# Optimization experiments

Hardware: AMD Instinct MI355X
Metric: run time of the kernel (lower is better)

The kernel has to match this reference:

```python
import jax, jax.numpy as jnp
import numpy as np

ITEM_NUM = 100000
EMBED = 128
HIDDEN = 256
BETA = 0.5
B = 4096
H = 200

def setup_inputs() -> dict:
    key = jax.random.key(0)
    ks = jax.random.split(key, 7)
    history = jax.random.randint(ks[0], (B, H), 0, ITEM_NUM)
    target = jax.random.randint(ks[1], (B,), 0, ITEM_NUM)
    embed_history = jax.random.normal(ks[2], (ITEM_NUM, EMBED), dtype=jnp.float32) * 0.01
    embed_target = jax.random.normal(ks[3], (ITEM_NUM, EMBED), dtype=jnp.float32) * 0.01
    # nn.Linear default init: U(-1/sqrt(fan_in), 1/sqrt(fan_in)); biases zeroed by _init_weight_
    lim1 = 1.0 / np.sqrt(EMBED)
    W1 = jax.random.uniform(ks[4], (EMBED, HIDDEN), dtype=jnp.float32, minval=-lim1, maxval=lim1)
    b1 = jnp.zeros((HIDDEN,), dtype=jnp.float32)
    lim2 = 1.0 / np.sqrt(HIDDEN)
    w2 = jax.random.uniform(ks[5], (HIDDEN,), dtype=jnp.float32, minval=-lim2, maxval=lim2)
    return {"history": history, "target": target, "embed_history": embed_history,
            "embed_target": embed_target, "W1": W1, "b1": b1, "w2": w2}

def reference(history, target, embed_history, embed_target, W1, b1, w2):
    hist_e = embed_history[history]            # [B, H, d]
    tgt_e = embed_target[target][:, None, :]   # [B, 1, d]
    x = hist_e * tgt_e                          # [B, H, d]
    a = jnp.einsum('bhk,k->bh', jax.nn.relu(jnp.einsum('bhd,dk->bhk', x, W1) + b1), w2)  # [B, H]
    mask = (history != target[:, None]).astype(a.dtype)  # [B, H]
    exp_A = jnp.exp(a) * mask                  # [B, H]
    denom = jnp.sum(exp_A, axis=-1) ** BETA    # [B], beta-power normalization (not softmax)
    attn = exp_A / denom[:, None]              # [B, H]
    pred = jnp.einsum('bh,bhd,bd->b', attn, hist_e, tgt_e[:, 0, :])  # [B]
    return jax.nn.sigmoid(pred)
```

## Files before the change

### kernel.cpp

```cpp
#include <hip/hip_runtime.h>

#define B_SZ   4096
#define H_SZ   200
#define D_SZ   128
#define N_SZ   256
#define ROWS   (B_SZ * H_SZ)
#define BM     64
#define TPB    8
#define RPB    (BM * TPB)
#define NBLK   (ROWS / RPB)

typedef _Float16 f16;
typedef __attribute__((ext_vector_type(2))) _Float16 f16x2;
typedef __attribute__((ext_vector_type(8))) _Float16 f16x8;
typedef __attribute__((ext_vector_type(4))) float f32x4;

union H8 { f16x8 v; f16x2 p[4]; uint4 u; };

__device__ __forceinline__ f16x2 pkrtz(float a, float b) {
    return __builtin_bit_cast(f16x2, __builtin_amdgcn_cvt_pkrtz(a, b));
}

__global__ __launch_bounds__(256) void cvt_eh(const float* __restrict__ src,
                                              uint4* __restrict__ dst, int n8) {
    int i = blockIdx.x * 256 + threadIdx.x;
    if (i >= n8) return;
    const f32x4* p = (const f32x4*)src + (size_t)i * 2;
    f32x4 a = p[0], b = p[1];
    uint4 o;
    o.x = __builtin_bit_cast(unsigned, pkrtz(a[0], a[1]));
    o.y = __builtin_bit_cast(unsigned, pkrtz(a[2], a[3]));
    o.z = __builtin_bit_cast(unsigned, pkrtz(b[0], b[1]));
    o.w = __builtin_bit_cast(unsigned, pkrtz(b[2], b[3]));
    dst[i] = o;
}

__global__ __launch_bounds__(256) void cvt_w1(const float* __restrict__ src,
                                              f16* __restrict__ dst) {
    int i = blockIdx.x * 256 + threadIdx.x;
    int n = i >> 7, d = i & 127;
    dst[i] = (f16)(src[d * N_SZ + n] * 0.0625f);
}

__global__ __launch_bounds__(512, 4) void nais_main(
    const int* __restrict__ history, const int* __restrict__ target,
    const uint4* __restrict__ ehh, const float* __restrict__ et,
    const f16* __restrict__ w1t, const float* __restrict__ b1,
    const float* __restrict__ w2,
    float* __restrict__ a_out, float* __restrict__ dotd_out)
{
    __shared__ uint4 AbufV[2][BM * 256 / 16];
    __shared__ float apart[2][8][BM];
    __shared__ f16   tgt_h[4][D_SZ];
    __shared__ int   tgt_i[4];

    const int tid  = threadIdx.x;
    const int wid  = tid >> 6;
    const int lane = tid & 63;
    const int lo   = lane & 15;
    const int hi   = lane >> 4;
    const int row  = tid >> 3;
    const int seg  = tid & 7;
    const int blk  = blockIdx.x;
    const int b_base = (blk * RPB) / H_SZ;

    if (tid < 4) {
        int bb = b_base + tid;
        tgt_i[tid] = target[bb < B_SZ ? bb : (B_SZ - 1)];
    }
    __syncthreads();
    if (tid < 256) {
        const int r4 = tid >> 6, j = (tid & 63) * 2;
        const float* src = et + (size_t)tgt_i[r4] * D_SZ + j;
        ((f16x2*)tgt_h)[tid] = pkrtz(src[0] * 16.f, src[1] * 16.f);
    }

    f16x8 wfrag[4][2];
    #pragma unroll
    for (int ni = 0; ni < 2; ++ni) {
        int n = 32 * wid + 16 * ni + lo;
        #pragma unroll
        for (int ki = 0; ki < 4; ++ki)
            wfrag[ki][ni] = *(const f16x8*)(w1t + (size_t)n * D_SZ + 32 * ki + 8 * hi);
    }
    const int n0 = 32 * wid + 4 * hi;
    const f32x4 b1a = *(const f32x4*)(b1 + n0);
    const f32x4 b1b = *(const f32x4*)(b1 + n0 + 16);
    const f32x4 w2a = *(const f32x4*)(w2 + n0);
    const f32x4 w2b = *(const f32x4*)(w2 + n0 + 16);

    const int grow0 = blk * RPB + row;
    const int* hrow = history + grow0;
    int ih_cur = hrow[0];
    int ih_nxt = hrow[BM];
    uint4 hq0, hq1;
    {
        const uint4* p = ehh + (size_t)ih_cur * 16;
        hq0 = p[seg]; hq1 = p[8 + seg];
    }
    int b_loc = grow0 / H_SZ - b_base;
    int rem   = grow0 - (b_loc + b_base) * H_SZ;
    __syncthreads();

    for (int t = 0; t < TPB; ++t) {
        char* Ab = (char*)AbufV[t & 1];
        const int gr = grow0 + t * BM;

        {
            H8 h1, h2, t1, t2, x1, x2;
            h1.u = hq0; h2.u = hq1;
            t1.v = *(const f16x8*)&tgt_h[b_loc][8 * seg];
            t2.v = *(const f16x8*)&tgt_h[b_loc][64 + 8 * seg];
            x1.v = h1.v * t1.v;
            x2.v = h2.v * t2.v;
            float s = 0.f;
            #pragma unroll
            for (int j = 0; j < 4; ++j) {
                s = __builtin_amdgcn_fdot2(h1.p[j], t1.p[j], s, false);
                s = __builtin_amdgcn_fdot2(h2.p[j], t2.p[j], s, false);
            }
            s += __shfl_xor(s, 1);
            s += __shfl_xor(s, 2);
            s += __shfl_xor(s, 4);
            if (seg == 0) dotd_out[gr] = s * 0.0625f;
            const unsigned sw = (unsigned)((row & 7) << 4);
            char* rb = Ab + row * 256;
            *(uint4*)(rb + (((unsigned)(16 * seg)) ^ sw))          = x1.u;
            *(uint4*)(rb + (128u + (((unsigned)(16 * seg)) ^ sw))) = x2.u;
        }
        __syncthreads();

        if (t + 1 < TPB) {
            ih_cur = ih_nxt;
            if (t + 2 < TPB) ih_nxt = hrow[(t + 2) * BM];
            const uint4* p = ehh + (size_t)ih_cur * 16;
            hq0 = p[seg]; hq1 = p[8 + seg];
        }

        if (t > 0 && tid < BM) {
            const float* ap = &apart[(t - 1) & 1][0][tid];
            float a = ap[0];
            #pragma unroll
            for (int w = 1; w < 8; ++w) a += ap[w * BM];
            a_out[blk * RPB + (t - 1) * BM + tid] = a;
        }

        #pragma unroll
        for (int mi = 0; mi < 4; ++mi) {
            const int rr = 16 * mi + lo;
            const unsigned swr = (unsigned)((rr & 7) << 4);
            f16x8 af[4];
            #pragma unroll
            for (int ki = 0; ki < 4; ++ki) {
                unsigned off = ((unsigned)(64 * ki + 16 * hi)) ^ swr;
                af[ki] = *(const f16x8*)(Ab + rr * 256 + off);
            }
            f32x4 acc0 = b1a;
            f32x4 acc1 = b1b;
            __builtin_amdgcn_s_setprio(1);
            #pragma unroll
            for (int ki = 0; ki < 4; ++ki) {
                acc0 = __builtin_amdgcn_mfma_f32_16x16x32_f16(wfrag[ki][0], af[ki], acc0, 0, 0, 0);
                acc1 = __builtin_amdgcn_mfma_f32_16x16x32_f16(wfrag[ki][1], af[ki], acc1, 0, 0, 0);
            }
            __builtin_amdgcn_s_setprio(0);
            float v = fmaxf(acc0[0], 0.f) * w2a[0] + fmaxf(acc1[0], 0.f) * w2b[0];
            v += fmaxf(acc0[1], 0.f) * w2a[1] + fmaxf(acc1[1], 0.f) * w2b[1];
            v += fmaxf(acc0[2], 0.f) * w2a[2] + fmaxf(acc1[2], 0.f) * w2b[2];
            v += fmaxf(acc0[3], 0.f) * w2a[3] + fmaxf(acc1[3], 0.f) * w2b[3];
            v += __shfl_xor(v, 16);
            v += __shfl_xor(v, 32);
            if (lane < 16) apart[t & 1][wid][16 * mi + lane] = v;
        }

        rem += BM;
        if (rem >= H_SZ) { rem -= H_SZ; ++b_loc; }
    }
    __syncthreads();
    if (tid < BM) {
        const float* ap = &apart[(TPB - 1) & 1][0][tid];
        float a = ap[0];
        #pragma unroll
        for (int w = 1; w < 8; ++w) a += ap[w * BM];
        a_out[blk * RPB + (TPB - 1) * BM + tid] = a;
    }
}

__global__ __launch_bounds__(64) void nais_finish(
    const int* __restrict__ history, const int* __restrict__ target,
    const float* __restrict__ a_in, const float* __restrict__ dotd_in,
    float* __restrict__ out)
{
    const int b    = blockIdx.x;
    const int lane = threadIdx.x;
    const int tgt  = target[b];
    float s1 = 0.f, s2 = 0.f;
    for (int h = lane; h < H_SZ; h += 64) {
        int rg = b * H_SZ + h;
        float e = (history[rg] != tgt) ? __expf(a_in[rg]) : 0.f;
        s1 += e;
        s2 += e * dotd_in[rg];
    }
    #pragma unroll
    for (int o = 1; o < 64; o <<= 1) {
        s1 += __shfl_xor(s1, o);
        s2 += __shfl_xor(s2, o);
    }
    if (lane == 0) {
        float pred = s2 / sqrtf(s1);
        out[b] = 1.f / (1.f + __expf(-pred));
    }
}

extern "C" void kernel_launch(void* const* d_in, const int* in_sizes, int n_in,
                              void* d_out, int out_size, void* d_ws, size_t ws_size,
                              hipStream_t stream) {
    const int*   history = (const int*)d_in[0];
    const int*   target  = (const int*)d_in[1];
    const float* eh      = (const float*)d_in[2];
    const float* et      = (const float*)d_in[3];
    const float* W1      = (const float*)d_in[4];
    const float* b1      = (const float*)d_in[5];
    const float* w2      = (const float*)d_in[6];
    float* out = (float*)d_out;

    char* ws = (char*)d_ws;
    uint4* ehh = (uint4*)ws;
    f16*   w1t = (f16*)(ws + (size_t)100000 * D_SZ * 2);
    float* a_ws = (float*)(ws + (size_t)100000 * D_SZ * 2 + N_SZ * D_SZ * 2);
    float* dotd_ws = a_ws + ROWS;

    const int n8 = 100000 * D_SZ / 8;
    cvt_eh<<<(n8 + 255) / 256, 256, 0, stream>>>(eh, ehh, n8);
    cvt_w1<<<(N_SZ * D_SZ) / 256, 256, 0, stream>>>(W1, w1t);
    nais_main<<<NBLK, 512, 0, stream>>>(history, target, ehh, et, w1t, b1, w2, a_ws, dotd_ws);
    nais_finish<<<B_SZ, 64, 0, stream>>>(history, target, a_ws, dotd_ws, out);
}
```

Baseline: 98.76 us.

## Halve block to 256 threads with each wave covering 64 hidden units

The main kernel now runs 256 threads (4 waves) per block instead of 512. Each wave computes 64 hidden columns with four MFMA accumulators instead of 32 with two, and each row's gather is split across 4 threads loading 64 bytes each instead of 8 threads. This means fewer waves share the same W1 fragments, a smaller cross-wave partial-sum reduction, and more MFMA work per A-fragment load from LDS. In exchange each wave holds twice the weight fragments in registers, and fewer threads are in flight to hide the embedding gather latency.

```diff
diff --git a/kernel.cpp b/kernel.cpp
--- a/kernel.cpp
+++ b/kernel.cpp
@@ -42,7 +42,7 @@
     dst[i] = (f16)(src[d * N_SZ + n] * 0.0625f);
 }
 
-__global__ __launch_bounds__(512, 4) void nais_main(
+__global__ __launch_bounds__(256, 3) void nais_main(
     const int* __restrict__ history, const int* __restrict__ target,
     const uint4* __restrict__ ehh, const float* __restrict__ et,
     const f16* __restrict__ w1t, const float* __restrict__ b1,
@@ -50,7 +50,7 @@
     float* __restrict__ a_out, float* __restrict__ dotd_out)
 {
     __shared__ uint4 AbufV[2][BM * 256 / 16];
-    __shared__ float apart[2][8][BM];
+    __shared__ float apart[2][4][BM];
     __shared__ f16   tgt_h[4][D_SZ];
     __shared__ int   tgt_i[4];
 
@@ -59,8 +59,8 @@
     const int lane = tid & 63;
     const int lo   = lane & 15;
     const int hi   = lane >> 4;
-    const int row  = tid >> 3;
-    const int seg  = tid & 7;
+    const int row  = tid >> 2;
+    const int seg  = tid & 3;
     const int blk  = blockIdx.x;
     const int b_base = (blk * RPB) / H_SZ;
 
@@ -69,34 +69,36 @@
         tgt_i[tid] = target[bb < B_SZ ? bb : (B_SZ - 1)];
     }
     __syncthreads();
-    if (tid < 256) {
+    {
         const int r4 = tid >> 6, j = (tid & 63) * 2;
         const float* src = et + (size_t)tgt_i[r4] * D_SZ + j;
         ((f16x2*)tgt_h)[tid] = pkrtz(src[0] * 16.f, src[1] * 16.f);
     }
 
-    f16x8 wfrag[4][2];
+    f16x8 wfrag[4][4];
     #pragma unroll
-    for (int ni = 0; ni < 2; ++ni) {
-        int n = 32 * wid + 16 * ni + lo;
+    for (int ni = 0; ni < 4; ++ni) {
+        int n = 64 * wid + 16 * ni + lo;
         #pragma unroll
         for (int ki = 0; ki < 4; ++ki)
             wfrag[ki][ni] = *(const f16x8*)(w1t + (size_t)n * D_SZ + 32 * ki + 8 * hi);
     }
-    const int n0 = 32 * wid + 4 * hi;
-    const f32x4 b1a = *(const f32x4*)(b1 + n0);
-    const f32x4 b1b = *(const f32x4*)(b1 + n0 + 16);
-    const f32x4 w2a = *(const f32x4*)(w2 + n0);
-    const f32x4 w2b = *(const f32x4*)(w2 + n0 + 16);
+    const int n0 = 64 * wid + 4 * hi;
+    f32x4 b1v[4], w2v[4];
+    #pragma unroll
+    for (int ni = 0; ni < 4; ++ni) {
+        b1v[ni] = *(const f32x4*)(b1 + n0 + 16 * ni);
+        w2v[ni] = *(const f32x4*)(w2 + n0 + 16 * ni);
+    }
 
     const int grow0 = blk * RPB + row;
     const int* hrow = history + grow0;
     int ih_cur = hrow[0];
     int ih_nxt = hrow[BM];
-    uint4 hq0, hq1;
+    uint4 hq0, hq1, hq2, hq3;
     {
-        const uint4* p = ehh + (size_t)ih_cur * 16;
-        hq0 = p[seg]; hq1 = p[8 + seg];
+        const uint4* p = ehh + (size_t)ih_cur * 16 + 4 * seg;
+        hq0 = p[0]; hq1 = p[1]; hq2 = p[2]; hq3 = p[3];
     }
     int b_loc = grow0 / H_SZ - b_base;
     int rem   = grow0 - (b_loc + b_base) * H_SZ;
@@ -107,41 +109,34 @@
         const int gr = grow0 + t * BM;
 
         {
-            H8 h1, h2, t1, t2, x1, x2;
-            h1.u = hq0; h2.u = hq1;
-            t1.v = *(const f16x8*)&tgt_h[b_loc][8 * seg];
-            t2.v = *(const f16x8*)&tgt_h[b_loc][64 + 8 * seg];
-            x1.v = h1.v * t1.v;
-            x2.v = h2.v * t2.v;
+            const f16x8* tp = (const f16x8*)&tgt_h[b_loc][32 * seg];
+            const unsigned sw = (unsigned)((row & 7) << 4);
+            char* rb = Ab + row * 256;
             float s = 0.f;
-            #pragma unroll
-            for (int j = 0; j < 4; ++j) {
-                s = __builtin_amdgcn_fdot2(h1.p[j], t1.p[j], s, false);
-                s = __builtin_amdgcn_fdot2(h2.p[j], t2.p[j], s, false);
-            }
+            #define CONS(J, HQ) { H8 h, tt, x; h.u = HQ; tt.v = tp[J]; x.v = h.v * tt.v; \
+                s = __builtin_amdgcn_fdot2(h.p[0], tt.p[0], s, false); \
+                s = __builtin_amdgcn_fdot2(h.p[1], tt.p[1], s, false); \
+                s = __builtin_amdgcn_fdot2(h.p[2], tt.p[2], s, false); \
+                s = __builtin_amdgcn_fdot2(h.p[3], tt.p[3], s, false); \
+                *(uint4*)(rb + (((unsigned)(64 * seg + 16 * J)) ^ sw)) = x.u; }
+            CONS(0, hq0) CONS(1, hq1) CONS(2, hq2) CONS(3, hq3)
+            #undef CONS
             s += __shfl_xor(s, 1);
             s += __shfl_xor(s, 2);
-            s += __shfl_xor(s, 4);
             if (seg == 0) dotd_out[gr] = s * 0.0625f;
-            const unsigned sw = (unsigned)((row & 7) << 4);
-            char* rb = Ab + row * 256;
-            *(uint4*)(rb + (((unsigned)(16 * seg)) ^ sw))          = x1.u;
-            *(uint4*)(rb + (128u + (((unsigned)(16 * seg)) ^ sw))) = x2.u;
         }
         __syncthreads();
 
         if (t + 1 < TPB) {
             ih_cur = ih_nxt;
             if (t + 2 < TPB) ih_nxt = hrow[(t + 2) * BM];
-            const uint4* p = ehh + (size_t)ih_cur * 16;
-            hq0 = p[seg]; hq1 = p[8 + seg];
+            const uint4* p = ehh + (size_t)ih_cur * 16 + 4 * seg;
+            hq0 = p[0]; hq1 = p[1]; hq2 = p[2]; hq3 = p[3];
         }
 
         if (t > 0 && tid < BM) {
             const float* ap = &apart[(t - 1) & 1][0][tid];
-            float a = ap[0];
-            #pragma unroll
-            for (int w = 1; w < 8; ++w) a += ap[w * BM];
+            float a = ap[0] + ap[BM] + ap[2 * BM] + ap[3 * BM];
             a_out[blk * RPB + (t - 1) * BM + tid] = a;
         }
 
@@ -155,19 +150,22 @@
                 unsigned off = ((unsigned)(64 * ki + 16 * hi)) ^ swr;
                 af[ki] = *(const f16x8*)(Ab + rr * 256 + off);
             }
-            f32x4 acc0 = b1a;
-            f32x4 acc1 = b1b;
+            f32x4 acc0 = b1v[0], acc1 = b1v[1], acc2 = b1v[2], acc3 = b1v[3];
             __builtin_amdgcn_s_setprio(1);
             #pragma unroll
             for (int ki = 0; ki < 4; ++ki) {
                 acc0 = __builtin_amdgcn_mfma_f32_16x16x32_f16(wfrag[ki][0], af[ki], acc0, 0, 0, 0);
                 acc1 = __builtin_amdgcn_mfma_f32_16x16x32_f16(wfrag[ki][1], af[ki], acc1, 0, 0, 0);
+                acc2 = __builtin_amdgcn_mfma_f32_16x16x32_f16(wfrag[ki][2], af[ki], acc2, 0, 0, 0);
+                acc3 = __builtin_amdgcn_mfma_f32_16x16x32_f16(wfrag[ki][3], af[ki], acc3, 0, 0, 0);
             }
             __builtin_amdgcn_s_setprio(0);
-            float v = fmaxf(acc0[0], 0.f) * w2a[0] + fmaxf(acc1[0], 0.f) * w2b[0];
-            v += fmaxf(acc0[1], 0.f) * w2a[1] + fmaxf(acc1[1], 0.f) * w2b[1];
-            v += fmaxf(acc0[2], 0.f) * w2a[2] + fmaxf(acc1[2], 0.f) * w2b[2];
-            v += fmaxf(acc0[3], 0.f) * w2a[3] + fmaxf(acc1[3], 0.f) * w2b[3];
+            float v = 0.f;
+            #define EPI(ACC, NI) \
+                v += fmaxf(ACC[0], 0.f) * w2v[NI][0] + fmaxf(ACC[1], 0.f) * w2v[NI][1] \
+                   + fmaxf(ACC[2], 0.f) * w2v[NI][2] + fmaxf(ACC[3], 0.f) * w2v[NI][3];
+            EPI(acc0, 0) EPI(acc1, 1) EPI(acc2, 2) EPI(acc3, 3)
+            #undef EPI
             v += __shfl_xor(v, 16);
             v += __shfl_xor(v, 32);
             if (lane < 16) apart[t & 1][wid][16 * mi + lane] = v;
@@ -179,9 +177,7 @@
     __syncthreads();
     if (tid < BM) {
         const float* ap = &apart[(TPB - 1) & 1][0][tid];
-        float a = ap[0];
-        #pragma unroll
-        for (int w = 1; w < 8; ++w) a += ap[w * BM];
+        float a = ap[0] + ap[BM] + ap[2 * BM] + ap[3 * BM];
         a_out[blk * RPB + (TPB - 1) * BM + tid] = a;
     }
 }
@@ -233,6 +229,6 @@
     const int n8 = 100000 * D_SZ / 8;
     cvt_eh<<<(n8 + 255) / 256, 256, 0, stream>>>(eh, ehh, n8);
     cvt_w1<<<(N_SZ * D_SZ) / 256, 256, 0, stream>>>(W1, w1t);
-    nais_main<<<NBLK, 512, 0, stream>>>(history, target, ehh, et, w1t, b1, w2, a_ws, dotd_ws);
+    nais_main<<<NBLK, 256, 0, stream>>>(history, target, ehh, et, w1t, b1, w2, a_ws, dotd_ws);
     nais_finish<<<B_SZ, 64, 0, stream>>>(history, target, a_ws, dotd_ws, out);
 }
```

Result: slower. 114.4 us (+15.8%).

## Retile MFMA warp layout to 2x4 grid over rows and hidden units

Applied to the files above, without the earlier changes.

Changes the per-wave split of the 64x256 hidden-layer GEMM from 8 waves each covering all 64 rows and 32 hidden units to a 2x4 grid where each wave covers 32 rows and 64 hidden units. Each A fragment loaded from LDS is now reused across four MFMAs instead of two, halving shared-memory reads of the activation tile, and the cross-wave partial-sum reduction drops from 8 to 4 terms. In exchange each wave holds twice as many W1 fragments and bias/w2 vectors in registers, so the occupancy hint is lowered from 4 to 3 blocks per CU.

```diff
diff --git a/kernel.cpp b/kernel.cpp
--- a/kernel.cpp
+++ b/kernel.cpp
@@ -42,7 +42,7 @@
     dst[i] = (f16)(src[d * N_SZ + n] * 0.0625f);
 }
 
-__global__ __launch_bounds__(512, 4) void nais_main(
+__global__ __launch_bounds__(512, 3) void nais_main(
     const int* __restrict__ history, const int* __restrict__ target,
     const uint4* __restrict__ ehh, const float* __restrict__ et,
     const f16* __restrict__ w1t, const float* __restrict__ b1,
@@ -50,7 +50,7 @@
     float* __restrict__ a_out, float* __restrict__ dotd_out)
 {
     __shared__ uint4 AbufV[2][BM * 256 / 16];
-    __shared__ float apart[2][8][BM];
+    __shared__ float apart[2][4][BM];
     __shared__ f16   tgt_h[4][D_SZ];
     __shared__ int   tgt_i[4];
 
@@ -59,6 +59,8 @@
     const int lane = tid & 63;
     const int lo   = lane & 15;
     const int hi   = lane >> 4;
+    const int wr   = wid >> 2;
+    const int wc   = wid & 3;
     const int row  = tid >> 3;
     const int seg  = tid & 7;
     const int blk  = blockIdx.x;
@@ -75,19 +77,21 @@
         ((f16x2*)tgt_h)[tid] = pkrtz(src[0] * 16.f, src[1] * 16.f);
     }
 
-    f16x8 wfrag[4][2];
+    f16x8 wfrag[4][4];
     #pragma unroll
-    for (int ni = 0; ni < 2; ++ni) {
-        int n = 32 * wid + 16 * ni + lo;
+    for (int ni = 0; ni < 4; ++ni) {
+        int n = 64 * wc + 16 * ni + lo;
         #pragma unroll
         for (int ki = 0; ki < 4; ++ki)
             wfrag[ki][ni] = *(const f16x8*)(w1t + (size_t)n * D_SZ + 32 * ki + 8 * hi);
     }
-    const int n0 = 32 * wid + 4 * hi;
-    const f32x4 b1a = *(const f32x4*)(b1 + n0);
-    const f32x4 b1b = *(const f32x4*)(b1 + n0 + 16);
-    const f32x4 w2a = *(const f32x4*)(w2 + n0);
-    const f32x4 w2b = *(const f32x4*)(w2 + n0 + 16);
+    const int n0 = 64 * wc + 4 * hi;
+    f32x4 b1v[4], w2v[4];
+    #pragma unroll
+    for (int ni = 0; ni < 4; ++ni) {
+        b1v[ni] = *(const f32x4*)(b1 + n0 + 16 * ni);
+        w2v[ni] = *(const f32x4*)(w2 + n0 + 16 * ni);
+    }
 
     const int grow0 = blk * RPB + row;
     const int* hrow = history + grow0;
@@ -139,15 +143,13 @@
 
         if (t > 0 && tid < BM) {
             const float* ap = &apart[(t - 1) & 1][0][tid];
-            float a = ap[0];
-            #pragma unroll
-            for (int w = 1; w < 8; ++w) a += ap[w * BM];
+            float a = ap[0] + ap[BM] + ap[2 * BM] + ap[3 * BM];
             a_out[blk * RPB + (t - 1) * BM + tid] = a;
         }
 
         #pragma unroll
-        for (int mi = 0; mi < 4; ++mi) {
-            const int rr = 16 * mi + lo;
+        for (int mi = 0; mi < 2; ++mi) {
+            const int rr = 32 * wr + 16 * mi + lo;
             const unsigned swr = (unsigned)((rr & 7) << 4);
             f16x8 af[4];
             #pragma unroll
@@ -155,22 +157,25 @@
                 unsigned off = ((unsigned)(64 * ki + 16 * hi)) ^ swr;
                 af[ki] = *(const f16x8*)(Ab + rr * 256 + off);
             }
-            f32x4 acc0 = b1a;
-            f32x4 acc1 = b1b;
+            f32x4 acc0 = b1v[0], acc1 = b1v[1], acc2 = b1v[2], acc3 = b1v[3];
             __builtin_amdgcn_s_setprio(1);
             #pragma unroll
             for (int ki = 0; ki < 4; ++ki) {
                 acc0 = __builtin_amdgcn_mfma_f32_16x16x32_f16(wfrag[ki][0], af[ki], acc0, 0, 0, 0);
                 acc1 = __builtin_amdgcn_mfma_f32_16x16x32_f16(wfrag[ki][1], af[ki], acc1, 0, 0, 0);
+                acc2 = __builtin_amdgcn_mfma_f32_16x16x32_f16(wfrag[ki][2], af[ki], acc2, 0, 0, 0);
+                acc3 = __builtin_amdgcn_mfma_f32_16x16x32_f16(wfrag[ki][3], af[ki], acc3, 0, 0, 0);
             }
             __builtin_amdgcn_s_setprio(0);
-            float v = fmaxf(acc0[0], 0.f) * w2a[0] + fmaxf(acc1[0], 0.f) * w2b[0];
-            v += fmaxf(acc0[1], 0.f) * w2a[1] + fmaxf(acc1[1], 0.f) * w2b[1];
-            v += fmaxf(acc0[2], 0.f) * w2a[2] + fmaxf(acc1[2], 0.f) * w2b[2];
-            v += fmaxf(acc0[3], 0.f) * w2a[3] + fmaxf(acc1[3], 0.f) * w2b[3];
+            float v = 0.f;
+            #define EPI(ACC, NI) \
+                v += fmaxf(ACC[0], 0.f) * w2v[NI][0] + fmaxf(ACC[1], 0.f) * w2v[NI][1] \
+                   + fmaxf(ACC[2], 0.f) * w2v[NI][2] + fmaxf(ACC[3], 0.f) * w2v[NI][3];
+            EPI(acc0, 0) EPI(acc1, 1) EPI(acc2, 2) EPI(acc3, 3)
+            #undef EPI
             v += __shfl_xor(v, 16);
             v += __shfl_xor(v, 32);
-            if (lane < 16) apart[t & 1][wid][16 * mi + lane] = v;
+            if (lane < 16) apart[t & 1][wc][32 * wr + 16 * mi + lane] = v;
         }
 
         rem += BM;
@@ -179,9 +184,7 @@
     __syncthreads();
     if (tid < BM) {
         const float* ap = &apart[(TPB - 1) & 1][0][tid];
-        float a = ap[0];
-        #pragma unroll
-        for (int w = 1; w < 8; ++w) a += ap[w * BM];
+        float a = ap[0] + ap[BM] + ap[2 * BM] + ap[3 * BM];
         a_out[blk * RPB + (TPB - 1) * BM + tid] = a;
     }
 }
```

Measured after the change: 122.3 us. 1.24x slower.

## Software-pipeline tile construction between MFMA phases with a single barrier per iteration

Applied to the files above, without the earlier changes.

Restructures the main loop so the next tile's x = h*t construction, its LDS store and the following gather prefetch are interleaved between the MFMA phases of the current tile. This removes one __syncthreads per iteration and moves the history index prefetch one step further ahead. The aim is to overlap global gather latency and VALU work with matrix-core work. It also drops the s_setprio hints and raises register pressure from the extra live values, which could hurt occupancy at the current launch bounds.

```diff
diff --git a/kernel.cpp b/kernel.cpp
--- a/kernel.cpp
+++ b/kernel.cpp
@@ -91,52 +91,90 @@
 
     const int grow0 = blk * RPB + row;
     const int* hrow = history + grow0;
-    int ih_cur = hrow[0];
-    int ih_nxt = hrow[BM];
     uint4 hq0, hq1;
     {
-        const uint4* p = ehh + (size_t)ih_cur * 16;
+        const uint4* p = ehh + (size_t)hrow[0] * 16;
         hq0 = p[seg]; hq1 = p[8 + seg];
     }
+    int ih_nxt = hrow[BM];
     int b_loc = grow0 / H_SZ - b_base;
     int rem   = grow0 - (b_loc + b_base) * H_SZ;
     __syncthreads();
 
+    #define CONSTRUCT(Bf, GR)                                                     \
+    {                                                                             \
+        H8 h1, h2, t1, t2, x1, x2;                                                \
+        h1.u = hq0; h2.u = hq1;                                                   \
+        t1.v = *(const f16x8*)&tgt_h[b_loc][8 * seg];                             \
+        t2.v = *(const f16x8*)&tgt_h[b_loc][64 + 8 * seg];                        \
+        x1.v = h1.v * t1.v;                                                       \
+        x2.v = h2.v * t2.v;                                                       \
+        float s = 0.f;                                                            \
+        _Pragma("unroll")                                                         \
+        for (int j = 0; j < 4; ++j) {                                             \
+            s = __builtin_amdgcn_fdot2(h1.p[j], t1.p[j], s, false);               \
+            s = __builtin_amdgcn_fdot2(h2.p[j], t2.p[j], s, false);               \
+        }                                                                         \
+        s += __shfl_xor(s, 1);                                                    \
+        s += __shfl_xor(s, 2);                                                    \
+        s += __shfl_xor(s, 4);                                                    \
+        if (seg == 0) dotd_out[GR] = s * 0.0625f;                                 \
+        const unsigned sw_ = (unsigned)((row & 7) << 4);                          \
+        char* rb_ = (char*)(Bf) + row * 256;                                      \
+        *(uint4*)(rb_ + (((unsigned)(16 * seg)) ^ sw_))          = x1.u;          \
+        *(uint4*)(rb_ + (128u + (((unsigned)(16 * seg)) ^ sw_))) = x2.u;          \
+    }
+
+    #define MIPHASE(Ab, MI, PAR)                                                  \
+    {                                                                             \
+        const int rr = 16 * (MI) + lo;                                            \
+        const unsigned swr = (unsigned)((rr & 7) << 4);                           \
+        f16x8 af[4];                                                              \
+        _Pragma("unroll")                                                         \
+        for (int ki = 0; ki < 4; ++ki) {                                          \
+            unsigned off = ((unsigned)(64 * ki + 16 * hi)) ^ swr;                 \
+            af[ki] = *(const f16x8*)((char*)(Ab) + rr * 256 + off);               \
+        }                                                                         \
+        f32x4 acc0 = b1a, acc1 = b1b;                                             \
+        _Pragma("unroll")                                                         \
+        for (int ki = 0; ki < 4; ++ki) {                                          \
+            acc0 = __builtin_amdgcn_mfma_f32_16x16x32_f16(wfrag[ki][0], af[ki], acc0, 0, 0, 0); \
+            acc1 = __builtin_amdgcn_mfma_f32_16x16x32_f16(wfrag[ki][1], af[ki], acc1, 0, 0, 0); \
+        }                                                                         \
+        float v = fmaxf(acc0[0], 0.f) * w2a[0] + fmaxf(acc1[0], 0.f) * w2b[0];    \
+        v += fmaxf(acc0[1], 0.f) * w2a[1] + fmaxf(acc1[1], 0.f) * w2b[1];         \
+        v += fmaxf(acc0[2], 0.f) * w2a[2] + fmaxf(acc1[2], 0.f) * w2b[2];         \
+        v += fmaxf(acc0[3], 0.f) * w2a[3] + fmaxf(acc1[3], 0.f) * w2b[3];         \
+        v += __shfl_xor(v, 16);                                                   \
+        v += __shfl_xor(v, 32);                                                   \
+        if (lane < 16) apart[PAR][wid][16 * (MI) + lane] = v;                     \
+    }
+
+    CONSTRUCT(AbufV[0], grow0)
+    {
+        const uint4* p = ehh + (size_t)ih_nxt * 16;
+        hq0 = p[seg]; hq1 = p[8 + seg];
+    }
+    ih_nxt = hrow[2 * BM];
+    __syncthreads();
+
     for (int t = 0; t < TPB; ++t) {
-        char* Ab = (char*)AbufV[t & 1];
-        const int gr = grow0 + t * BM;
-
-        {
-            H8 h1, h2, t1, t2, x1, x2;
-            h1.u = hq0; h2.u = hq1;
-            t1.v = *(const f16x8*)&tgt_h[b_loc][8 * seg];
-            t2.v = *(const f16x8*)&tgt_h[b_loc][64 + 8 * seg];
-            x1.v = h1.v * t1.v;
-            x2.v = h2.v * t2.v;
-            float s = 0.f;
-            #pragma unroll
-            for (int j = 0; j < 4; ++j) {
-                s = __builtin_amdgcn_fdot2(h1.p[j], t1.p[j], s, false);
-                s = __builtin_amdgcn_fdot2(h2.p[j], t2.p[j], s, false);
+        const uint4* Ab = AbufV[t & 1];
+        const int par = t & 1;
+
+        MIPHASE(Ab, 0, par)
+        MIPHASE(Ab, 1, par)
+
+        if (t + 1 < TPB) {
+            rem += BM;
+            if (rem >= H_SZ) { rem -= H_SZ; ++b_loc; }
+            CONSTRUCT(AbufV[(t + 1) & 1], grow0 + (t + 1) * BM)
+            if (t + 2 < TPB) {
+                const uint4* p = ehh + (size_t)ih_nxt * 16;
+                hq0 = p[seg]; hq1 = p[8 + seg];
             }
-            s += __shfl_xor(s, 1);
-            s += __shfl_xor(s, 2);
-            s += __shfl_xor(s, 4);
-            if (seg == 0) dotd_out[gr] = s * 0.0625f;
-            const unsigned sw = (unsigned)((row & 7) << 4);
-            char* rb = Ab + row * 256;
-            *(uint4*)(rb + (((unsigned)(16 * seg)) ^ sw))          = x1.u;
-            *(uint4*)(rb + (128u + (((unsigned)(16 * seg)) ^ sw))) = x2.u;
+            if (t + 3 < TPB) ih_nxt = hrow[(t + 3) * BM];
         }
-        __syncthreads();
-
-        if (t + 1 < TPB) {
-            ih_cur = ih_nxt;
-            if (t + 2 < TPB) ih_nxt = hrow[(t + 2) * BM];
-            const uint4* p = ehh + (size_t)ih_cur * 16;
-            hq0 = p[seg]; hq1 = p[8 + seg];
-        }
-
         if (t > 0 && tid < BM) {
             const float* ap = &apart[(t - 1) & 1][0][tid];
             float a = ap[0];
@@ -145,38 +183,11 @@
             a_out[blk * RPB + (t - 1) * BM + tid] = a;
         }
 
-        #pragma unroll
-        for (int mi = 0; mi < 4; ++mi) {
-            const int rr = 16 * mi + lo;
-            const unsigned swr = (unsigned)((rr & 7) << 4);
-            f16x8 af[4];
-            #pragma unroll
-            for (int ki = 0; ki < 4; ++ki) {
-                unsigned off = ((unsigned)(64 * ki + 16 * hi)) ^ swr;
-                af[ki] = *(const f16x8*)(Ab + rr * 256 + off);
-            }
-            f32x4 acc0 = b1a;
-            f32x4 acc1 = b1b;
-            __builtin_amdgcn_s_setprio(1);
-            #pragma unroll
-            for (int ki = 0; ki < 4; ++ki) {
-                acc0 = __builtin_amdgcn_mfma_f32_16x16x32_f16(wfrag[ki][0], af[ki], acc0, 0, 0, 0);
-                acc1 = __builtin_amdgcn_mfma_f32_16x16x32_f16(wfrag[ki][1], af[ki], acc1, 0, 0, 0);
-            }
-            __builtin_amdgcn_s_setprio(0);
-            float v = fmaxf(acc0[0], 0.f) * w2a[0] + fmaxf(acc1[0], 0.f) * w2b[0];
-            v += fmaxf(acc0[1], 0.f) * w2a[1] + fmaxf(acc1[1], 0.f) * w2b[1];
-            v += fmaxf(acc0[2], 0.f) * w2a[2] + fmaxf(acc1[2], 0.f) * w2b[2];
-            v += fmaxf(acc0[3], 0.f) * w2a[3] + fmaxf(acc1[3], 0.f) * w2b[3];
-            v += __shfl_xor(v, 16);
-            v += __shfl_xor(v, 32);
-            if (lane < 16) apart[t & 1][wid][16 * mi + lane] = v;
-        }
-
-        rem += BM;
-        if (rem >= H_SZ) { rem -= H_SZ; ++b_loc; }
-    }
-    __syncthreads();
+        MIPHASE(Ab, 2, par)
+        MIPHASE(Ab, 3, par)
+
+        __syncthreads();
+    }
     if (tid < BM) {
         const float* ap = &apart[(TPB - 1) & 1][0][tid];
         float a = ap[0];
@@ -184,6 +195,8 @@
         for (int w = 1; w < 8; ++w) a += ap[w * BM];
         a_out[blk * RPB + (TPB - 1) * BM + tid] = a;
     }
+    #undef CONSTRUCT
+    #undef MIPHASE
 }
 
 __global__ __launch_bounds__(64) void nais_finish(
```

After: 101.1 us. +2.4%, slower.
